# Kernel optimization log

Measured on AMD Instinct MI355X. Metric: run time of the kernel, lower is better.

Reference implementation:

```python
import jax, jax.numpy as jnp
import numpy as np
import math

B, T, C, NH, NL, AD, V, BS, MT = 32, 50, 128, 8, 6, 64, 18, 150, 4096
HD = C // NH


def setup_inputs():
    key = jax.random.key(0)
    ks = jax.random.split(key, 32)
    w = lambda i, shape, s=0.02: (jax.random.normal(ks[i], shape) * s).astype(jnp.float32)
    d = {}
    d["states"] = jax.random.uniform(ks[0], (B, T, 4, 84, 84), jnp.float32)
    d["rtgs"] = jax.random.normal(ks[1], (B, T, 1), jnp.float32)
    d["actions"] = jax.random.randint(ks[2], (B, T, 1), 0, V)
    d["timesteps"] = jax.random.randint(ks[3], (B, 1, 1), 0, MT)
    d["targets"] = jax.random.randint(ks[4], (B, T, 1), 0, V)
    d["pos_emb"] = w(5, (1, BS + 1, C))
    d["global_pos_emb"] = w(6, (1, MT + 1, C))
    d["c1_w"] = w(7, (32, 4, 8, 8)); d["c1_b"] = w(8, (32,), 0.01)
    d["c2_w"] = w(9, (64, 32, 4, 4)); d["c2_b"] = w(10, (64,), 0.01)
    d["c3_w"] = w(11, (64, 64, 3, 3)); d["c3_b"] = w(12, (64,), 0.01)
    d["enc_w"] = w(13, (C, 3136)); d["enc_b"] = w(14, (C,), 0.01)
    d["ret_w"] = w(15, (C, 1)); d["ret_b"] = w(16, (C,), 0.01)
    d["act_tab"] = w(17, (V, C))
    d["ln_w"] = jnp.ones((NL, 3, C), jnp.float32)
    d["ln_b"] = jnp.zeros((NL, 3, C), jnp.float32)
    d["attn_w"] = w(18, (NL, 4, C, C)); d["attn_b"] = w(19, (NL, 4, C), 0.01)
    d["mlp_w1"] = w(20, (NL, 4 * C, C)); d["mlp_b1"] = w(21, (NL, 4 * C), 0.01)
    d["mlp_w2"] = w(22, (NL, C, 4 * C)); d["mlp_b2"] = w(23, (NL, C), 0.01)
    d["ad_dw"] = w(24, (NL, AD, C), 1e-3); d["ad_db"] = jnp.zeros((NL, AD), jnp.float32)
    d["ad_uw"] = w(25, (NL, C, AD), 1e-3); d["ad_ub"] = jnp.zeros((NL, C), jnp.float32)
    d["lnf_w"] = jnp.ones((C,), jnp.float32); d["lnf_b"] = jnp.zeros((C,), jnp.float32)
    d["head_w"] = w(26, (V, C))
    return d


def _ln(x, g, b):
    m = jnp.mean(x, -1, keepdims=True)
    v = jnp.mean(jnp.square(x - m), -1, keepdims=True)
    return (x - m) * jax.lax.rsqrt(v + 1e-5) * g + b


def _conv(x, w, b, s):
    y = jax.lax.conv_general_dilated(x, w, (s, s), "VALID", dimension_numbers=("NCHW", "OIHW", "NCHW"))
    return y + b[None, :, None, None]


def _forward(states, rtgs, pos_emb, global_pos_emb, c1_w, c1_b, c2_w, c2_b, c3_w, c3_b,
             enc_w, enc_b, ret_w, ret_b, act_tab, ln_w, ln_b, attn_w, attn_b,
             mlp_w1, mlp_b1, mlp_w2, mlp_b2, ad_dw, ad_db, ad_uw, ad_ub,
             lnf_w, lnf_b, head_w, actions, timesteps):
    # state encoder (conv stem): [B*T,4,84,84] -> [B,T,C]
    x = states.reshape(-1, 4, 84, 84)
    x = jax.nn.relu(_conv(x, c1_w, c1_b, 4))  # -> 20x20
    x = jax.nn.relu(_conv(x, c2_w, c2_b, 2))  # -> 9x9
    x = jax.nn.relu(_conv(x, c3_w, c3_b, 1))  # -> 7x7
    x = x.reshape(x.shape[0], -1)             # 64*7*7 = 3136
    state_e = jnp.tanh(x @ enc_w.T + enc_b).reshape(B, T, C)
    rtg_e = jnp.tanh(rtgs @ ret_w.T + ret_b)
    act_e = jnp.tanh(act_tab[actions[..., 0]])
    # interleave rtg/state/action at [::3],[1::3],[2::3]
    tok = jnp.stack([rtg_e, state_e, act_e], axis=2).reshape(B, 3 * T, C)
    S = 3 * T
    pe = global_pos_emb[0][timesteps[:, 0, 0]][:, None, :] + pos_emb[:, :S, :]
    h = tok + pe  # drop = identity in eval
    mask = jnp.tril(jnp.ones((S, S), bool))
    scale = 1.0 / math.sqrt(HD)
    for l in range(NL):
        normed = _ln(h, ln_w[l, 2], ln_b[l, 2])           # ln3 on pre-block input
        xa = _ln(h, ln_w[l, 0], ln_b[l, 0])               # ln1
        k = (xa @ attn_w[l, 0].T + attn_b[l, 0]).reshape(B, S, NH, HD)
        q = (xa @ attn_w[l, 1].T + attn_b[l, 1]).reshape(B, S, NH, HD)
        v = (xa @ attn_w[l, 2].T + attn_b[l, 2]).reshape(B, S, NH, HD)
        att = jnp.einsum("bihd,bjhd->bhij", q, k) * scale
        att = jax.nn.softmax(jnp.where(mask, att, -jnp.inf), axis=-1)
        y = jnp.einsum("bhij,bjhd->bihd", att, v).reshape(B, S, C)
        h1 = h + y @ attn_w[l, 3].T + attn_b[l, 3]
        xm = _ln(h1, ln_w[l, 1], ln_b[l, 1])              # ln2
        f = h1 + jax.nn.gelu(xm @ mlp_w1[l].T + mlp_b1[l], approximate=False) @ mlp_w2[l].T + mlp_b2[l]
        ad = jax.nn.relu(normed @ ad_dw[l].T + ad_db[l]) @ ad_uw[l].T + ad_ub[l]
        h = h1 + f + ad                                   # x = hidden + drop(forward) + adapter
    logits = _ln(h, lnf_w, lnf_b) @ head_w.T
    return logits[:, 1::3, :]  # predictions from state tokens


def reference(states, rtgs, pos_emb, global_pos_emb, c1_w, c1_b, c2_w, c2_b, c3_w, c3_b,
              enc_w, enc_b, ret_w, ret_b, act_tab, ln_w, ln_b, attn_w, attn_b,
              mlp_w1, mlp_b1, mlp_w2, mlp_b2, ad_dw, ad_db, ad_uw, ad_ub,
              lnf_w, lnf_b, head_w, actions, timesteps, targets):
    # targets only toggles sequence layout (not None here) and the CE loss; logits are the kernel payload
    return _forward(states, rtgs, pos_emb, global_pos_emb, c1_w, c1_b, c2_w, c2_b, c3_w, c3_b,
                    enc_w, enc_b, ret_w, ret_b, act_tab, ln_w, ln_b, attn_w, attn_b,
                    mlp_w1, mlp_b1, mlp_w2, mlp_b2, ad_dw, ad_db, ad_uw, ad_ub,
                    lnf_w, lnf_b, head_w, actions, timesteps)
```

## Files before the change

kernel.cpp:

```cpp
#include <hip/hip_runtime.h>
#include <hip/hip_bf16.h>
#include <math.h>

typedef __hip_bfloat16 bf16;

typedef __attribute__((ext_vector_type(8))) short bfrag;
typedef __attribute__((ext_vector_type(4))) float f32x4;
union FragU { bfrag s; uint2 d[2]; unsigned int u[4]; };

static __device__ __forceinline__ float b2f(bf16 x){ return __bfloat162float(x); }
static __device__ __forceinline__ float2 upk2(unsigned int u){
  union { unsigned int i; float f; } a, b;
  a.i = u << 16;
  b.i = u & 0xffff0000u;
  float2 r; r.x = a.f; r.y = b.f; return r;
}
static __device__ __forceinline__ unsigned int f2b2(float lo, float hi){
  bf16 l = __float2bfloat16(lo), h = __float2bfloat16(hi);
  unsigned short lb, hb;
  __builtin_memcpy(&lb, &l, 2); __builtin_memcpy(&hb, &h, 2);
  return (unsigned int)lb | ((unsigned int)hb << 16);
}
static __device__ __forceinline__ void sto(float* p, size_t i, float v){ p[i] = v; }
static __device__ __forceinline__ void sto(bf16* p, size_t i, float v){ p[i] = __float2bfloat16(v); }

constexpr size_t MiB = 1ull << 20;
constexpr size_t OFF_C1   = 0;
constexpr size_t OFF_C2   = 41*MiB;
constexpr size_t OFF_C3   = 58*MiB;
constexpr size_t OFF_SE   = 69*MiB;
constexpr size_t OFF_H    = 0;
constexpr size_t OFF_XA   = 3*MiB;
constexpr size_t OFF_NORM = 6*MiB;
constexpr size_t OFF_QKV  = 9*MiB;
constexpr size_t OFF_Y    = 17*MiB;
constexpr size_t OFF_H1   = 20*MiB;
constexpr size_t OFF_MLPH = 23*MiB;
constexpr size_t OFF_ADH  = 33*MiB;
constexpr size_t OFF_WT   = 0;

__global__ __launch_bounds__(256) void conv1_kernel(
    const float* __restrict__ x, const float* __restrict__ w,
    const float* __restrict__ bias, bf16* __restrict__ out)
{
  __shared__ bf16 xs1[4*84*88];
  int b = blockIdx.x;
  int t = threadIdx.x;
  const float4* xb4 = (const float4*)(x + (size_t)b*28224);
  for (int e = t; e < 7056; e += 256){
    int c = e / 1764, rem = e % 1764;
    int r = rem / 21, c4 = (rem % 21)*4;
    float4 f = xb4[e];
    *(uint2*)(xs1 + (c*84 + r)*88 + c4) = make_uint2(f2b2(f.x, f.y), f2b2(f.z, f.w));
  }
  __syncthreads();
  int lane = t & 63, wave = t >> 6;
  int quad = lane >> 4, r16 = lane & 15;
  f32x4 acc[7][2];
  #pragma unroll
  for (int i = 0; i < 7; ++i)
    #pragma unroll
    for (int j = 0; j < 2; ++j) acc[i][j] = (f32x4){0.f,0.f,0.f,0.f};
  for (int kc = 0; kc < 8; ++kc){
    int c = kc >> 1, ky = (kc & 1)*4 + quad;
    FragU bf_[2];
    #pragma unroll
    for (int tn = 0; tn < 2; ++tn){
      int oc = tn*16 + r16;
      const float* wp = w + oc*256 + kc*32 + quad*8;
      float4 wa = ((const float4*)wp)[0], wb = ((const float4*)wp)[1];
      bf_[tn].u[0] = f2b2(wa.x, wa.y); bf_[tn].u[1] = f2b2(wa.z, wa.w);
      bf_[tn].u[2] = f2b2(wb.x, wb.y); bf_[tn].u[3] = f2b2(wb.z, wb.w);
    }
    #pragma unroll
    for (int i = 0; i < 7; ++i){
      int tile = wave*7 + i;
      if (tile < 25){
        int m = tile*16 + r16;
        int oy = m / 20, ox = m % 20;
        const bf16* p = xs1 + ((c*84 + 4*oy + ky)*88 + 4*ox);
        FragU a;
        a.d[0] = *(const uint2*)p;
        a.d[1] = *(const uint2*)(p + 4);
        acc[i][0] = __builtin_amdgcn_mfma_f32_16x16x32_bf16(a.s, bf_[0].s, acc[i][0], 0, 0, 0);
        acc[i][1] = __builtin_amdgcn_mfma_f32_16x16x32_bf16(a.s, bf_[1].s, acc[i][1], 0, 0, 0);
      }
    }
  }
  __syncthreads();
  #pragma unroll
  for (int i = 0; i < 7; ++i){
    int tile = wave*7 + i;
    if (tile < 25){
      int m0 = tile*16 + quad*4;
      #pragma unroll
      for (int tn = 0; tn < 2; ++tn){
        int oc = tn*16 + r16;
        float bb = bias[oc];
        float v0 = fmaxf(acc[i][tn][0] + bb, 0.f);
        float v1 = fmaxf(acc[i][tn][1] + bb, 0.f);
        float v2 = fmaxf(acc[i][tn][2] + bb, 0.f);
        float v3 = fmaxf(acc[i][tn][3] + bb, 0.f);
        *(uint2*)(xs1 + oc*408 + m0) = make_uint2(f2b2(v0, v1), f2b2(v2, v3));
      }
    }
  }
  __syncthreads();
  bf16* outp = out + (size_t)b*12800;
  for (int e = t; e < 1600; e += 256){
    int oc = e / 50, col = e % 50;
    uint4 v = *(const uint4*)(xs1 + oc*408 + col*8);
    *(uint4*)(outp + oc*400 + col*8) = v;
  }
}

__global__ __launch_bounds__(256) void conv2_kernel(
    const bf16* __restrict__ x, const float* __restrict__ w,
    const float* __restrict__ bias, bf16* __restrict__ out)
{
  __shared__ bf16 xs2[32*20*24];
  int b = blockIdx.x;
  int t = threadIdx.x;
  const unsigned int* xb = (const unsigned int*)(x + (size_t)b*12800);
  for (int p = t; p < 6400; p += 256){
    int c = p / 200, rem = p % 200;
    int r = rem / 10, cp = rem % 10;
    ((unsigned int*)xs2)[((c*20 + r)*24 + 2*cp) >> 1] = xb[p];
  }
  __syncthreads();
  int lane = t & 63, wave = t >> 6;
  int quad = lane >> 4, r16 = lane & 15;
  int oc = wave*16 + r16;
  f32x4 acc[6];
  #pragma unroll
  for (int i = 0; i < 6; ++i) acc[i] = (f32x4){0.f,0.f,0.f,0.f};
  for (int kc = 0; kc < 16; ++kc){
    const float* wp = w + oc*512 + kc*32 + quad*8;
    float4 wa = ((const float4*)wp)[0], wb = ((const float4*)wp)[1];
    FragU bfr;
    bfr.u[0] = f2b2(wa.x, wa.y); bfr.u[1] = f2b2(wa.z, wa.w);
    bfr.u[2] = f2b2(wb.x, wb.y); bfr.u[3] = f2b2(wb.z, wb.w);
    int c = kc*2 + (quad >> 1);
    int ky0 = (quad & 1)*2;
    #pragma unroll
    for (int tile = 0; tile < 6; ++tile){
      int m = tile*16 + r16; if (m > 80) m = 80;
      int oy = m / 9, ox = m % 9;
      int idx1 = (c*20 + 2*oy + ky0)*24 + 2*ox;
      const unsigned int* q1 = (const unsigned int*)(xs2 + idx1);
      const unsigned int* q2 = (const unsigned int*)(xs2 + idx1 + 24);
      FragU a;
      a.u[0] = q1[0]; a.u[1] = q1[1];
      a.u[2] = q2[0]; a.u[3] = q2[1];
      acc[tile] = __builtin_amdgcn_mfma_f32_16x16x32_bf16(a.s, bfr.s, acc[tile], 0, 0, 0);
    }
  }
  __syncthreads();
  float bb = bias[oc];
  #pragma unroll
  for (int tile = 0; tile < 6; ++tile){
    #pragma unroll
    for (int r = 0; r < 4; ++r){
      int m = tile*16 + quad*4 + r;
      if (m < 81){
        float v = fmaxf(acc[tile][r] + bb, 0.f);
        xs2[oc*81 + m] = __float2bfloat16(v);
      }
    }
  }
  __syncthreads();
  const unsigned int* lsu = (const unsigned int*)xs2;
  unsigned int* op = (unsigned int*)(out + (size_t)b*5184);
  for (int e = t; e < 2592; e += 256) op[e] = lsu[e];
}

__global__ __launch_bounds__(256) void wt_kernel(const float* __restrict__ w, bf16* __restrict__ wt)
{
  int o = blockIdx.x*256 + threadIdx.x;
  int oc = o / 576, r = o % 576;
  int tap = r >> 6, c = r & 63;
  wt[o] = __float2bfloat16(w[oc*576 + c*9 + tap]);
}

__global__ __launch_bounds__(256) void conv3_kernel(
    const bf16* __restrict__ x, const bf16* __restrict__ wt,
    const float* __restrict__ bias, bf16* __restrict__ out)
{
  __shared__ ushort lin[5184];
  __shared__ ushort xt[81*72];
  int b = blockIdx.x;
  int t = threadIdx.x;
  const uint2* xb = (const uint2*)(x + (size_t)b*5184);
  for (int i = t; i < 1296; i += 256) ((uint2*)lin)[i] = xb[i];
  __syncthreads();
  for (int e = t; e < 5184; e += 256){
    int c = e & 63, p = e >> 6;
    xt[p*72 + c] = lin[c*81 + p];
  }
  __syncthreads();
  int lane = t & 63, wv = t >> 6;
  int quad = lane >> 4, r16 = lane & 15;
  int m = wv*16 + r16;
  int pos = m < 49 ? m : 48;
  int pb = (pos/7)*9 + (pos%7);
  const ushort* abase = xt + pb*72 + quad*8;
  const bf16* wb0 = wt + (size_t)r16*576 + quad*8;
  f32x4 acc[4];
  #pragma unroll
  for (int tn = 0; tn < 4; ++tn) acc[tn] = (f32x4){0.f,0.f,0.f,0.f};
  #pragma unroll 3
  for (int kc = 0; kc < 18; ++kc){
    int tap = kc >> 1;
    int toff = (tap/3)*9 + (tap%3);
    int soff = toff*72 + (kc & 1)*32;
    FragU a;
    uint4 av = *(const uint4*)(abase + soff);
    a.u[0] = av.x; a.u[1] = av.y; a.u[2] = av.z; a.u[3] = av.w;
    #pragma unroll
    for (int tn = 0; tn < 4; ++tn){
      uint4 bv = *(const uint4*)(wb0 + tn*9216 + kc*32);
      FragU bfr;
      bfr.u[0] = bv.x; bfr.u[1] = bv.y; bfr.u[2] = bv.z; bfr.u[3] = bv.w;
      acc[tn] = __builtin_amdgcn_mfma_f32_16x16x32_bf16(a.s, bfr.s, acc[tn], 0, 0, 0);
    }
  }
  __syncthreads();
  #pragma unroll
  for (int tn = 0; tn < 4; ++tn){
    int oc = tn*16 + r16;
    float bb = bias[oc];
    #pragma unroll
    for (int r = 0; r < 4; ++r){
      int p = wv*16 + quad*4 + r;
      if (p < 49){
        bf16 v = __float2bfloat16(fmaxf(acc[tn][r] + bb, 0.f));
        ushort u; __builtin_memcpy(&u, &v, 2);
        lin[oc*49 + p] = u;
      }
    }
  }
  __syncthreads();
  uint2* op = (uint2*)(out + (size_t)b*3136);
  for (int e = t; e < 784; e += 256) op[e] = ((const uint2*)lin)[e];
}

template<int ACT, typename OT>
__global__ __launch_bounds__(256) void mgemm(
    const bf16* __restrict__ X, const float* __restrict__ W,
    const float* __restrict__ bias, const float* __restrict__ add, float add_scale,
    OT* __restrict__ out, int M, int N, int K)
{
  __shared__ bf16 Xs[64*40];
  __shared__ bf16 Ws[64*40];
  int nb = N >> 6;
  int bn = (blockIdx.x % nb) << 6;
  int bm = (blockIdx.x / nb) << 6;
  int t = threadIdx.x;
  int lane = t & 63, wave = t >> 6;
  int mw = wave >> 1, nw = wave & 1;
  int quad = lane >> 4, r16 = lane & 15;
  int srow = t >> 2, scol = (t & 3)*8;
  f32x4 acc[2][2];
  #pragma unroll
  for (int i = 0; i < 2; ++i)
    #pragma unroll
    for (int j = 0; j < 2; ++j) acc[i][j] = (f32x4){0.f,0.f,0.f,0.f};
  for (int k0 = 0; k0 < K; k0 += 32){
    uint4 xv = *(const uint4*)(X + (size_t)(bm + srow)*K + k0 + scol);
    uint2* xd = (uint2*)(Xs + srow*40 + scol);
    xd[0] = make_uint2(xv.x, xv.y); xd[1] = make_uint2(xv.z, xv.w);
    const float* wp = W + (size_t)(bn + srow)*K + k0 + scol;
    float4 wa = ((const float4*)wp)[0], wb = ((const float4*)wp)[1];
    uint2* wd = (uint2*)(Ws + srow*40 + scol);
    wd[0] = make_uint2(f2b2(wa.x, wa.y), f2b2(wa.z, wa.w));
    wd[1] = make_uint2(f2b2(wb.x, wb.y), f2b2(wb.z, wb.w));
    __syncthreads();
    FragU af[2], bf_[2];
    #pragma unroll
    for (int tm = 0; tm < 2; ++tm){
      const bf16* p = Xs + (mw*32 + tm*16 + r16)*40 + quad*8;
      af[tm].d[0] = *(const uint2*)p; af[tm].d[1] = *(const uint2*)(p + 4);
    }
    #pragma unroll
    for (int tn = 0; tn < 2; ++tn){
      const bf16* p = Ws + (nw*32 + tn*16 + r16)*40 + quad*8;
      bf_[tn].d[0] = *(const uint2*)p; bf_[tn].d[1] = *(const uint2*)(p + 4);
    }
    #pragma unroll
    for (int tm = 0; tm < 2; ++tm)
      #pragma unroll
      for (int tn = 0; tn < 2; ++tn)
        acc[tm][tn] = __builtin_amdgcn_mfma_f32_16x16x32_bf16(af[tm].s, bf_[tn].s, acc[tm][tn], 0, 0, 0);
    __syncthreads();
  }
  #pragma unroll
  for (int tm = 0; tm < 2; ++tm){
    #pragma unroll
    for (int tn = 0; tn < 2; ++tn){
      int n = bn + nw*32 + tn*16 + r16;
      float bb = bias[n];
      #pragma unroll
      for (int r = 0; r < 4; ++r){
        int m = bm + mw*32 + tm*16 + quad*4 + r;
        float v = acc[tm][tn][r] + bb;
        if (ACT == 1) v = tanhf(v);
        else if (ACT == 2) v = 0.5f*v*(1.0f + erff(v*0.70710678118f));
        else if (ACT == 3) v = fmaxf(v, 0.f);
        if (add) v += add_scale * add[(size_t)m*N + n];
        sto(out, (size_t)m*N + n, v);
      }
    }
  }
}

__global__ __launch_bounds__(256) void token_kernel(
    const float* __restrict__ rtgs, const int* __restrict__ actions, const int* __restrict__ timesteps,
    const float* __restrict__ ret_w, const float* __restrict__ ret_b, const float* __restrict__ act_tab,
    const float* __restrict__ pos_emb, const float* __restrict__ gpe,
    const float* __restrict__ se, float* __restrict__ h)
{
  int idx = blockIdx.x*256 + threadIdx.x;
  int c = idx & 127; int row = idx >> 7;
  int s = row % 150; int b = row / 150;
  int t = s / 3; int r = s - 3*t;
  float tok;
  if (r == 0)      tok = tanhf(rtgs[b*50+t] * ret_w[c] + ret_b[c]);
  else if (r == 1) tok = se[(b*50+t)*128 + c];
  else             tok = tanhf(act_tab[actions[b*50+t]*128 + c]);
  float pe = gpe[(size_t)timesteps[b]*128 + c] + pos_emb[s*128 + c];
  h[idx] = tok + pe;
}

__global__ __launch_bounds__(256) void ln_kernel(
    const float* __restrict__ x,
    const float* __restrict__ g1, const float* __restrict__ be1, bf16* __restrict__ o1,
    const float* __restrict__ g2, const float* __restrict__ be2, bf16* o2)
{
  int lane = threadIdx.x & 63;
  int row = blockIdx.x*4 + (threadIdx.x >> 6);
  const float2 xv = *(const float2*)(x + (size_t)row*128 + lane*2);
  float s = xv.x + xv.y, sq = xv.x*xv.x + xv.y*xv.y;
  #pragma unroll
  for (int off = 32; off; off >>= 1){ s += __shfl_xor(s, off); sq += __shfl_xor(sq, off); }
  float mean = s * 0.0078125f;
  float var  = sq * 0.0078125f - mean*mean;
  float rstd = rsqrtf(var + 1e-5f);
  float n0 = (xv.x - mean)*rstd, n1 = (xv.y - mean)*rstd;
  int c0 = lane*2;
  ((unsigned int*)o1)[row*64 + lane] = f2b2(n0*g1[c0] + be1[c0], n1*g1[c0+1] + be1[c0+1]);
  if (o2)
    ((unsigned int*)o2)[row*64 + lane] = f2b2(n0*g2[c0] + be2[c0], n1*g2[c0+1] + be2[c0+1]);
}

__global__ __launch_bounds__(256) void attn_kernel(const bf16* __restrict__ qkv, bf16* __restrict__ y)
{
  int bh = blockIdx.x;
  int hh = bh & 7; int b = bh >> 3;
  __shared__ float ks[150*16];
  __shared__ float vs[150*16];
  int t = threadIdx.x;
  for (int i = t; i < 2400; i += 256){
    int s = i >> 4; int d = i & 15;
    const bf16* base = qkv + (size_t)(b*150 + s)*384;
    ks[i] = b2f(base[hh*16 + d]);
    vs[i] = b2f(base[256 + hh*16 + d]);
  }
  __syncthreads();
  if (t < 150){
    const bf16* qr = qkv + (size_t)(b*150 + t)*384 + 128 + hh*16;
    float q[16];
    #pragma unroll
    for (int d = 0; d < 16; ++d) q[d] = b2f(qr[d]) * 0.25f;
    float m = -1e30f, l = 0.f, acc[16] = {};
    for (int j = 0; j <= t; ++j){
      const float* kr = ks + j*16;
      float s = 0.f;
      #pragma unroll
      for (int d = 0; d < 16; ++d) s += q[d]*kr[d];
      float mn = fmaxf(m, s);
      float corr = __expf(m - mn);
      float p = __expf(s - mn);
      l = l*corr + p;
      const float* vr = vs + j*16;
      #pragma unroll
      for (int d = 0; d < 16; ++d) acc[d] = acc[d]*corr + p*vr[d];
      m = mn;
    }
    float inv = 1.f / l;
    bf16* yr = y + (size_t)(b*150 + t)*128 + hh*16;
    #pragma unroll
    for (int d = 0; d < 16; ++d) yr[d] = __float2bfloat16(acc[d]*inv);
  }
}

__global__ __launch_bounds__(64) void head_kernel(
    const float* __restrict__ h, const float* __restrict__ g, const float* __restrict__ be,
    const float* __restrict__ hw, float* __restrict__ out)
{
  int bt = blockIdx.x;
  int lane = threadIdx.x;
  int b = bt / 50, t = bt % 50;
  const float* row = h + ((size_t)b*150 + 3*t + 1)*128;
  float2 xv = *(const float2*)(row + lane*2);
  float s = xv.x + xv.y, sq = xv.x*xv.x + xv.y*xv.y;
  #pragma unroll
  for (int off = 32; off; off >>= 1){ s += __shfl_xor(s, off); sq += __shfl_xor(sq, off); }
  float mean = s * 0.0078125f;
  float var  = sq * 0.0078125f - mean*mean;
  float rstd = rsqrtf(var + 1e-5f);
  int c0 = lane*2;
  __shared__ float sh[128];
  sh[c0]   = (xv.x-mean)*rstd*g[c0]   + be[c0];
  sh[c0+1] = (xv.y-mean)*rstd*g[c0+1] + be[c0+1];
  __syncthreads();
  if (lane < 18){
    const float* wr = hw + lane*128;
    float acc = 0.f;
    #pragma unroll
    for (int c = 0; c < 128; c += 4){
      float4 wf = *(const float4*)(wr + c);
      acc += sh[c]*wf.x + sh[c+1]*wf.y + sh[c+2]*wf.z + sh[c+3]*wf.w;
    }
    out[bt*18 + lane] = acc;
  }
}

extern "C" void kernel_launch(void* const* d_in, const int* in_sizes, int n_in,
                              void* d_out, int out_size, void* d_ws, size_t ws_size,
                              hipStream_t stream)
{
  const float* states    = (const float*)d_in[0];
  const float* rtgs      = (const float*)d_in[1];
  const int*   actions   = (const int*)d_in[2];
  const int*   timesteps = (const int*)d_in[3];
  const float* pos_emb   = (const float*)d_in[5];
  const float* gpe       = (const float*)d_in[6];
  const float* c1_w = (const float*)d_in[7];  const float* c1_b = (const float*)d_in[8];
  const float* c2_w = (const float*)d_in[9];  const float* c2_b = (const float*)d_in[10];
  const float* c3_w = (const float*)d_in[11]; const float* c3_b = (const float*)d_in[12];
  const float* enc_w = (const float*)d_in[13]; const float* enc_b = (const float*)d_in[14];
  const float* ret_w = (const float*)d_in[15]; const float* ret_b = (const float*)d_in[16];
  const float* act_tab = (const float*)d_in[17];
  const float* ln_w = (const float*)d_in[18]; const float* ln_b = (const float*)d_in[19];
  const float* attn_w = (const float*)d_in[20]; const float* attn_b = (const float*)d_in[21];
  const float* mlp_w1 = (const float*)d_in[22]; const float* mlp_b1 = (const float*)d_in[23];
  const float* mlp_w2 = (const float*)d_in[24]; const float* mlp_b2 = (const float*)d_in[25];
  const float* ad_dw = (const float*)d_in[26]; const float* ad_db = (const float*)d_in[27];
  const float* ad_uw = (const float*)d_in[28]; const float* ad_ub = (const float*)d_in[29];
  const float* lnf_w = (const float*)d_in[30]; const float* lnf_b = (const float*)d_in[31];
  const float* head_w = (const float*)d_in[32];
  float* out = (float*)d_out;

  char* ws = (char*)d_ws;
  bf16* c1o  = (bf16*)(ws + OFF_C1);
  bf16* c2o  = (bf16*)(ws + OFF_C2);
  bf16* c3o  = (bf16*)(ws + OFF_C3);
  float* se  = (float*)(ws + OFF_SE);
  float* h   = (float*)(ws + OFF_H);
  bf16* xa   = (bf16*)(ws + OFF_XA);
  bf16* nrm  = (bf16*)(ws + OFF_NORM);
  bf16* qkv  = (bf16*)(ws + OFF_QKV);
  bf16* y    = (bf16*)(ws + OFF_Y);
  float* h1  = (float*)(ws + OFF_H1);
  bf16* mlph = (bf16*)(ws + OFF_MLPH);
  bf16* adh  = (bf16*)(ws + OFF_ADH);
  bf16* wtb  = (bf16*)(ws + OFF_WT);

  conv1_kernel<<<1600, 256, 0, stream>>>(states, c1_w, c1_b, c1o);
  conv2_kernel<<<1600, 256, 0, stream>>>(c1o, c2_w, c2_b, c2o);
  wt_kernel<<<144, 256, 0, stream>>>(c3_w, wtb);
  conv3_kernel<<<1600, 256, 0, stream>>>(c2o, wtb, c3_b, c3o);
  mgemm<1, float><<<25*2, 256, 0, stream>>>(c3o, enc_w, enc_b, nullptr, 0.f, se, 1600, 128, 3136);
  token_kernel<<<2400, 256, 0, stream>>>(rtgs, actions, timesteps, ret_w, ret_b, act_tab,
                                         pos_emb, gpe, se, h);

  for (int l = 0; l < 6; ++l){
    const float* g1 = ln_w + (l*3+0)*128; const float* be1 = ln_b + (l*3+0)*128;
    const float* g2 = ln_w + (l*3+1)*128; const float* be2 = ln_b + (l*3+1)*128;
    const float* g3 = ln_w + (l*3+2)*128; const float* be3 = ln_b + (l*3+2)*128;
    ln_kernel<<<1200, 256, 0, stream>>>(h, g1, be1, xa, g3, be3, nrm);
    mgemm<0, bf16><<<75*6, 256, 0, stream>>>(xa, attn_w + (size_t)l*4*16384, attn_b + l*4*128,
                                             nullptr, 0.f, qkv, 4800, 384, 128);
    attn_kernel<<<256, 256, 0, stream>>>(qkv, y);
    mgemm<0, float><<<75*2, 256, 0, stream>>>(y, attn_w + ((size_t)l*4+3)*16384, attn_b + (l*4+3)*128,
                                              h, 1.0f, h1, 4800, 128, 128);
    ln_kernel<<<1200, 256, 0, stream>>>(h1, g2, be2, xa, nullptr, nullptr, nullptr);
    mgemm<2, bf16><<<75*8, 256, 0, stream>>>(xa, mlp_w1 + (size_t)l*65536, mlp_b1 + l*512,
                                             nullptr, 0.f, mlph, 4800, 512, 128);
    mgemm<3, bf16><<<75*1, 256, 0, stream>>>(nrm, ad_dw + (size_t)l*8192, ad_db + l*64,
                                             nullptr, 0.f, adh, 4800, 64, 128);
    mgemm<0, float><<<75*2, 256, 0, stream>>>(mlph, mlp_w2 + (size_t)l*65536, mlp_b2 + l*128,
                                              h1, 2.0f, h, 4800, 128, 512);
    mgemm<0, float><<<75*2, 256, 0, stream>>>(adh, ad_uw + (size_t)l*8192, ad_ub + l*128,
                                              h, 1.0f, h, 4800, 128, 64);
  }
  head_kernel<<<1600, 64, 0, stream>>>(h, lnf_w, lnf_b, head_w, out);
}
```

Before: 1.109 ms.

## Read conv1 inputs directly from global memory and pre-convert weights to bf16

Conv1 no longer stages the whole 4x84x84 frame into LDS as bf16. Each lane now loads its own float4 pairs from global memory and converts them to bf16 in registers, and the LDS buffer shrinks to the output-staging size, which should raise occupancy. A small new kernel converts the conv1 weights to bf16 once, so each block stops re-converting them from float. The tradeoff is uncached, strided global reads repeated across overlapping 8x8 windows (stride 4) in place of reuse through LDS.

```diff
diff --git a/kernel.cpp b/kernel.cpp
--- a/kernel.cpp
+++ b/kernel.cpp
@@ -9,12 +9,6 @@
 union FragU { bfrag s; uint2 d[2]; unsigned int u[4]; };
 
 static __device__ __forceinline__ float b2f(bf16 x){ return __bfloat162float(x); }
-static __device__ __forceinline__ float2 upk2(unsigned int u){
-  union { unsigned int i; float f; } a, b;
-  a.i = u << 16;
-  b.i = u & 0xffff0000u;
-  float2 r; r.x = a.f; r.y = b.f; return r;
-}
 static __device__ __forceinline__ unsigned int f2b2(float lo, float hi){
   bf16 l = __float2bfloat16(lo), h = __float2bfloat16(hi);
   unsigned short lb, hb;
@@ -38,24 +32,32 @@
 constexpr size_t OFF_MLPH = 23*MiB;
 constexpr size_t OFF_ADH  = 33*MiB;
 constexpr size_t OFF_WT   = 0;
+constexpr size_t OFF_WT1  = OFF_C2;
+
+__global__ __launch_bounds__(256) void c1wt_kernel(const float* __restrict__ w, bf16* __restrict__ wt)
+{
+  int i = blockIdx.x*256 + threadIdx.x;
+  wt[i] = __float2bfloat16(w[i]);
+}
 
 __global__ __launch_bounds__(256) void conv1_kernel(
-    const float* __restrict__ x, const float* __restrict__ w,
+    const float* __restrict__ x, const bf16* __restrict__ wt,
     const float* __restrict__ bias, bf16* __restrict__ out)
 {
-  __shared__ bf16 xs1[4*84*88];
+  __shared__ bf16 ost[32*408];
   int b = blockIdx.x;
   int t = threadIdx.x;
-  const float4* xb4 = (const float4*)(x + (size_t)b*28224);
-  for (int e = t; e < 7056; e += 256){
-    int c = e / 1764, rem = e % 1764;
-    int r = rem / 21, c4 = (rem % 21)*4;
-    float4 f = xb4[e];
-    *(uint2*)(xs1 + (c*84 + r)*88 + c4) = make_uint2(f2b2(f.x, f.y), f2b2(f.z, f.w));
-  }
-  __syncthreads();
   int lane = t & 63, wave = t >> 6;
   int quad = lane >> 4, r16 = lane & 15;
+  const float* xb = x + (size_t)b*28224;
+  const float* pb[7];
+  #pragma unroll
+  for (int i = 0; i < 7; ++i){
+    int tile = wave*7 + i; if (tile > 24) tile = 24;
+    int m = tile*16 + r16;
+    int oy = m / 20, ox = m % 20;
+    pb[i] = xb + 4*oy*84 + 4*ox;
+  }
   f32x4 acc[7][2];
   #pragma unroll
   for (int i = 0; i < 7; ++i)
@@ -63,31 +65,27 @@
     for (int j = 0; j < 2; ++j) acc[i][j] = (f32x4){0.f,0.f,0.f,0.f};
   for (int kc = 0; kc < 8; ++kc){
     int c = kc >> 1, ky = (kc & 1)*4 + quad;
+    int off = c*7056 + ky*84;
     FragU bf_[2];
     #pragma unroll
     for (int tn = 0; tn < 2; ++tn){
-      int oc = tn*16 + r16;
-      const float* wp = w + oc*256 + kc*32 + quad*8;
-      float4 wa = ((const float4*)wp)[0], wb = ((const float4*)wp)[1];
-      bf_[tn].u[0] = f2b2(wa.x, wa.y); bf_[tn].u[1] = f2b2(wa.z, wa.w);
-      bf_[tn].u[2] = f2b2(wb.x, wb.y); bf_[tn].u[3] = f2b2(wb.z, wb.w);
+      uint4 wv = *(const uint4*)(wt + (tn*16 + r16)*256 + kc*32 + quad*8);
+      bf_[tn].u[0] = wv.x; bf_[tn].u[1] = wv.y; bf_[tn].u[2] = wv.z; bf_[tn].u[3] = wv.w;
     }
     #pragma unroll
     for (int i = 0; i < 7; ++i){
-      int tile = wave*7 + i;
-      if (tile < 25){
-        int m = tile*16 + r16;
-        int oy = m / 20, ox = m % 20;
-        const bf16* p = xs1 + ((c*84 + 4*oy + ky)*88 + 4*ox);
+      if (wave*7 + i < 25){
+        const float* p = pb[i] + off;
+        float4 fa = *(const float4*)p;
+        float4 fb = *(const float4*)(p + 4);
         FragU a;
-        a.d[0] = *(const uint2*)p;
-        a.d[1] = *(const uint2*)(p + 4);
+        a.u[0] = f2b2(fa.x, fa.y); a.u[1] = f2b2(fa.z, fa.w);
+        a.u[2] = f2b2(fb.x, fb.y); a.u[3] = f2b2(fb.z, fb.w);
         acc[i][0] = __builtin_amdgcn_mfma_f32_16x16x32_bf16(a.s, bf_[0].s, acc[i][0], 0, 0, 0);
         acc[i][1] = __builtin_amdgcn_mfma_f32_16x16x32_bf16(a.s, bf_[1].s, acc[i][1], 0, 0, 0);
       }
     }
   }
-  __syncthreads();
   #pragma unroll
   for (int i = 0; i < 7; ++i){
     int tile = wave*7 + i;
@@ -101,7 +99,7 @@
         float v1 = fmaxf(acc[i][tn][1] + bb, 0.f);
         float v2 = fmaxf(acc[i][tn][2] + bb, 0.f);
         float v3 = fmaxf(acc[i][tn][3] + bb, 0.f);
-        *(uint2*)(xs1 + oc*408 + m0) = make_uint2(f2b2(v0, v1), f2b2(v2, v3));
+        *(uint2*)(ost + oc*408 + m0) = make_uint2(f2b2(v0, v1), f2b2(v2, v3));
       }
     }
   }
@@ -109,7 +107,7 @@
   bf16* outp = out + (size_t)b*12800;
   for (int e = t; e < 1600; e += 256){
     int oc = e / 50, col = e % 50;
-    uint4 v = *(const uint4*)(xs1 + oc*408 + col*8);
+    uint4 v = *(const uint4*)(ost + oc*408 + col*8);
     *(uint4*)(outp + oc*400 + col*8) = v;
   }
 }
@@ -465,8 +463,10 @@
   bf16* mlph = (bf16*)(ws + OFF_MLPH);
   bf16* adh  = (bf16*)(ws + OFF_ADH);
   bf16* wtb  = (bf16*)(ws + OFF_WT);
-
-  conv1_kernel<<<1600, 256, 0, stream>>>(states, c1_w, c1_b, c1o);
+  bf16* wt1  = (bf16*)(ws + OFF_WT1);
+
+  c1wt_kernel<<<32, 256, 0, stream>>>(c1_w, wt1);
+  conv1_kernel<<<1600, 256, 0, stream>>>(states, wt1, c1_b, c1o);
   conv2_kernel<<<1600, 256, 0, stream>>>(c1o, c2_w, c2_b, c2o);
   wt_kernel<<<144, 256, 0, stream>>>(c3_w, wtb);
   conv3_kernel<<<1600, 256, 0, stream>>>(c2o, wtb, c3_b, c3o);
```

New measurement: 1.087 ms. No clear change (-2.0%).
